# Performance work log

Measured on AMD Instinct MI355X. Metric: run time of the kernel, lower is better.

The kernel has to match this reference:

```python
import jax, jax.numpy as jnp
import numpy as np

DIM_M = 512
NEG_INF = -1e30


def setup_inputs() -> dict:
    key = jax.random.key(0)
    k1, k2, k3, k4, k5, k6, k7 = jax.random.split(key, 7)
    B, Lc, Lq, d = 16, 1024, 512, DIM_M
    C = jax.random.normal(k1, (B, Lc, d), dtype=jnp.float32)
    Q = jax.random.normal(k2, (B, Lq, d), dtype=jnp.float32)
    cmask = jax.random.randint(k3, (B, Lc), 0, 2).astype(jnp.float32)
    qmask = jax.random.randint(k4, (B, Lq), 0, 2).astype(jnp.float32)
    lim = np.sqrt(1.0 / d)
    w = jax.random.uniform(k5, (3 * d,), minval=-lim, maxval=lim, dtype=jnp.float32)
    # out_linear: Linear(4d -> d), torch default init
    bound = np.sqrt(1.0 / (4 * d))
    out_w = jax.random.uniform(k6, (d, 4 * d), minval=-bound, maxval=bound, dtype=jnp.float32)
    out_b = jax.random.uniform(k7, (d,), minval=-bound, maxval=bound, dtype=jnp.float32)
    return {"C": C, "Q": Q, "cmask": cmask, "qmask": qmask, "w": w, "out_w": out_w, "out_b": out_b}


def _mask_logits(t, m):
    return t * m + (1.0 - m) * NEG_INF


def reference(C, Q, cmask, qmask, w, out_w, out_b):
    d = C.shape[-1]
    w1, w2, w3 = w[:d], w[d:2 * d], w[2 * d:]
    # Decomposed trilinear similarity (same math as cat([Ct,Qt,Ct*Qt]) @ w):
    # S[b,i,j] = C[b,i]@w1 + Q[b,j]@w2 + (C[b,i]*w3) @ Q[b,j]
    S = (C @ w1)[:, :, None] + (Q @ w2)[:, None, :] \
        + jnp.einsum('bid,bjd->bij', C * w3, Q)  # [B, Lc, Lq]
    qm = qmask[:, None, :]  # [B, 1, Lq]
    cm = cmask[:, :, None]  # [B, Lc, 1]
    S1 = jax.nn.softmax(_mask_logits(S, qm), axis=2)  # over Lq
    S2 = jax.nn.softmax(_mask_logits(S, cm), axis=1)  # over Lc
    A = jnp.einsum('bij,bjd->bid', S1, Q)  # [B, Lc, d]
    # bmm(bmm(S1, S2^T), C) == S1 @ (S2^T @ C) by associativity (cheaper)
    S2TC = jnp.einsum('bij,bid->bjd', S2, C)  # [B, Lq, d]
    Bm = jnp.einsum('bij,bjd->bid', S1, S2TC)  # [B, Lc, d]
    out = jnp.concatenate([C, A, C * A, C * Bm], axis=2)  # [B, Lc, 4d]
    # dropout inactive (inference); out_linear
    return out @ out_w.T + out_b
```

## Files before the change

kernel.cpp:

```cpp
#include <hip/hip_runtime.h>
#include <hip/hip_bf16.h>


#define NB 16
#define LC 1024
#define LQ 512
#define DM 512
#define D4 2048
#define NEGINF (-1e30f)

typedef __bf16 v8bf __attribute__((ext_vector_type(8)));
typedef __bf16 v4bf __attribute__((ext_vector_type(4)));
typedef float  v4f  __attribute__((ext_vector_type(4)));

#define MFMA16 __builtin_amdgcn_mfma_f32_16x16x32_bf16

#define GLOAD16(gp, lp) __builtin_amdgcn_global_load_lds( \
    (const __attribute__((address_space(1))) void*)(gp), \
    (__attribute__((address_space(3))) void*)(lp), 16, 0, 0)

__device__ __forceinline__ void xcd_remap(int& bx, int& by, int& bz) {
  const int gx = gridDim.x, gy = gridDim.y, gz = gridDim.z;
  int flat = bx + gx * (by + gy * bz);
  int per = (gx * gy * gz) >> 3;
  int nw = (flat & 7) * per + (flat >> 3);
  bx = nw % gx;
  int r = nw / gx;
  by = r % gy;
  bz = r / gy;
}

#define P_PROLOG \
  __shared__ __bf16 Al[4][128 * 32], Bl[4][64 * 32]; \
  int bx = blockIdx.x, by = blockIdx.y, bz = blockIdx.z; \
  xcd_remap(bx, by, bz); \
  const int b = bz, i0 = by * 128, n0 = bx * 64; \
  const int t = threadIdx.x, lane = t & 63, wave = t >> 6; \
  const int wm = wave >> 1, wn = wave & 1, quad = lane >> 4, col = lane & 15; \
  const int srA = wave * 32 + (lane >> 2); \
  const int srB = wave * 16 + (lane >> 2); \
  const int swz = (((lane & 3) ^ ((lane >> 2) & 3) ^ ((lane >> 4) & 3)) * 8); \
  const int rdx = ((quad ^ (col & 3) ^ ((col >> 2) & 3)) * 8); \
  v4f acc[4][2]; \
  _Pragma("unroll") for (int x = 0; x < 4; ++x) \
  _Pragma("unroll") for (int y = 0; y < 2; ++y) \
  _Pragma("unroll") for (int r = 0; r < 4; ++r) acc[x][y][r] = 0.f;

#define P_STAGE1(s, Aptr, Bptr, LDGA, LDGB, k0) \
  do { \
    GLOAD16((Aptr) + (k0),                       &Al[s][(wave * 32) * 32]); \
    GLOAD16((Aptr) + (size_t)16 * (LDGA) + (k0), &Al[s][(wave * 32 + 16) * 32]); \
    GLOAD16((Bptr) + (k0),                       &Bl[s][(wave * 16) * 32]); \
  } while (0)

#define P_COMPUTE(buf) \
  do { \
    v8bf af_[4], bf_[2]; \
    _Pragma("unroll") for (int x = 0; x < 4; ++x) \
      af_[x] = *(const v8bf*)&Al[buf][(wm * 64 + x * 16 + col) * 32 + rdx]; \
    _Pragma("unroll") for (int y = 0; y < 2; ++y) \
      bf_[y] = *(const v8bf*)&Bl[buf][(wn * 32 + y * 16 + col) * 32 + rdx]; \
    _Pragma("unroll") for (int x = 0; x < 4; ++x) \
    _Pragma("unroll") for (int y = 0; y < 2; ++y) \
      acc[x][y] = MFMA16(af_[x], bf_[y], acc[x][y], 0, 0, 0); \
  } while (0)

#define P_KLOOP(Arow, Brow, LDGA, LDGB, KEXT) \
  { P_STAGE1(0, Arow, Brow, LDGA, LDGB, 0); \
    P_STAGE1(1, Arow, Brow, LDGA, LDGB, 32); \
    const int np_ = (KEXT) / 64; \
    for (int q = 0; q < np_; ++q) { \
      asm volatile("s_waitcnt vmcnt(0)" ::: "memory"); \
      __builtin_amdgcn_s_barrier(); \
      const int s0_ = (2 * q) & 3, s1_ = s0_ + 1; \
      if (q + 1 < np_) { \
        const int t0_ = (2 * q + 2) & 3, t1_ = t0_ + 1; \
        P_STAGE1(t0_, Arow, Brow, LDGA, LDGB, (q + 1) * 64); \
        P_STAGE1(t1_, Arow, Brow, LDGA, LDGB, (q + 1) * 64 + 32); \
      } \
      P_COMPUTE(s0_); \
      P_COMPUTE(s1_); \
    } }

#define O_PROLOG \
  __shared__ __bf16 Al[3][128 * 32], Bl[3][128 * 32]; \
  int bx = blockIdx.x, by = blockIdx.y, bz = blockIdx.z; \
  xcd_remap(bx, by, bz); \
  const int b = bz, i0 = by * 128, n0 = bx * 128; \
  const int t = threadIdx.x, lane = t & 63, wave = t >> 6; \
  const int wm = wave >> 1, wn = wave & 1, quad = lane >> 4, col = lane & 15; \
  const int sr32 = wave * 32 + (lane >> 2); \
  const int swz = (((lane & 3) ^ ((lane >> 2) & 3) ^ ((lane >> 4) & 3)) * 8); \
  const int rdx = ((quad ^ (col & 3) ^ ((col >> 2) & 3)) * 8); \
  v4f acc[4][4]; \
  _Pragma("unroll") for (int x = 0; x < 4; ++x) \
  _Pragma("unroll") for (int y = 0; y < 4; ++y) \
  _Pragma("unroll") for (int r = 0; r < 4; ++r) acc[x][y][r] = 0.f;

#define O_STAGE(buf, Aptr, Bptr, LDGA, LDGB, k0) \
  do { \
    GLOAD16((Aptr) + (k0),                       &Al[buf][(wave * 32) * 32]); \
    GLOAD16((Aptr) + (size_t)16 * (LDGA) + (k0), &Al[buf][(wave * 32 + 16) * 32]); \
    GLOAD16((Bptr) + (k0),                       &Bl[buf][(wave * 32) * 32]); \
    GLOAD16((Bptr) + (size_t)16 * (LDGB) + (k0), &Bl[buf][(wave * 32 + 16) * 32]); \
  } while (0)

#define O_COMPUTE(buf) \
  do { \
    v8bf af_[4], bf_[4]; \
    _Pragma("unroll") for (int x = 0; x < 4; ++x) \
      af_[x] = *(const v8bf*)&Al[buf][(wm * 64 + x * 16 + col) * 32 + rdx]; \
    _Pragma("unroll") for (int y = 0; y < 4; ++y) \
      bf_[y] = *(const v8bf*)&Bl[buf][(wn * 64 + y * 16 + col) * 32 + rdx]; \
    __builtin_amdgcn_s_setprio(1); \
    _Pragma("unroll") for (int x = 0; x < 4; ++x) \
    _Pragma("unroll") for (int y = 0; y < 4; ++y) \
      acc[x][y] = MFMA16(af_[x], bf_[y], acc[x][y], 0, 0, 0); \
    __builtin_amdgcn_s_setprio(0); \
  } while (0)

#define O_SYNC4() \
  do { asm volatile("s_waitcnt vmcnt(4)" ::: "memory"); \
       __builtin_amdgcn_s_barrier(); } while (0)
#define O_SYNC0() \
  do { asm volatile("s_waitcnt vmcnt(0)" ::: "memory"); \
       __builtin_amdgcn_s_barrier(); } while (0)

#define O_ROT() do { cur_ = (cur_ == 2) ? 0 : cur_ + 1; \
                     nx2_ = (nx2_ == 2) ? 0 : nx2_ + 1; } while (0)

__global__ void k_rowdots(const float* __restrict__ C, const float* __restrict__ Q,
                          const float* __restrict__ w,
                          float* __restrict__ cw1, float* __restrict__ qw2,
                          __bf16* __restrict__ Cbf, __bf16* __restrict__ Qw3) {
  const int wid = threadIdx.x >> 6, lane = threadIdx.x & 63;
  const int row = blockIdx.x * 4 + wid;
  const bool isC = row < NB * LC;
  const int lr = isC ? row : row - NB * LC;
  const float* src = (isC ? C : Q) + (size_t)lr * DM;
  const float* wv  = isC ? w : (w + DM);
  const float* w3  = w + 2 * DM;
  __bf16* dst = (isC ? Cbf : Qw3) + (size_t)lr * DM;
  float v = 0.f;
#pragma unroll
  for (int s = 0; s < 2; ++s) {
    const int k = lane * 4 + s * 256;
    float4 f = *(const float4*)(src + k);
    float4 g = *(const float4*)(wv + k);
    v += f.x * g.x + f.y * g.y + f.z * g.z + f.w * g.w;
    v4bf h;
    if (isC) {
      h[0] = (__bf16)f.x; h[1] = (__bf16)f.y; h[2] = (__bf16)f.z; h[3] = (__bf16)f.w;
    } else {
      float4 s3 = *(const float4*)(w3 + k);
      h[0] = (__bf16)(f.x * s3.x); h[1] = (__bf16)(f.y * s3.y);
      h[2] = (__bf16)(f.z * s3.z); h[3] = (__bf16)(f.w * s3.w);
    }
    *(v4bf*)(dst + k) = h;
  }
#pragma unroll
  for (int off = 32; off; off >>= 1) v += __shfl_down(v, off, 64);
  if (lane == 0) {
    if (isC) cw1[row] = v;
    else     qw2[lr] = v;
  }
}

__device__ __forceinline__ void transpose_tile_f32(const float* __restrict__ in,
                                                   __bf16* __restrict__ outT,
                                                   int R, int Cd, int tbx, int tby, int tb) {
  __shared__ __bf16 tile[64][66];
  const int r0 = tby * 64, c0 = tbx * 64;
  const int tr = threadIdx.x >> 6, tc = threadIdx.x & 63;
  const float* inb = in + (size_t)tb * R * Cd;
  __bf16* outb = outT + (size_t)tb * Cd * R;
  for (int r = tr; r < 64; r += 4)
    tile[r][tc] = (__bf16)inb[(size_t)(r0 + r) * Cd + c0 + tc];
  __syncthreads();
  for (int c = tr; c < 64; c += 4)
    outb[(size_t)(c0 + c) * R + r0 + tc] = tile[tc][c];
}

__device__ __forceinline__ void transpose_tile_bf(const __bf16* __restrict__ in,
                                                  __bf16* __restrict__ outT,
                                                  int R, int Cd, int tbx, int tby, int tb) {
  __shared__ __bf16 tile[64][66];
  const int r0 = tby * 64, c0 = tbx * 64;
  const int tr = threadIdx.x >> 6, tc = threadIdx.x & 63;
  const __bf16* inb = in + (size_t)tb * R * Cd;
  __bf16* outb = outT + (size_t)tb * Cd * R;
  for (int r = tr; r < 64; r += 4)
    tile[r][tc] = inb[(size_t)(r0 + r) * Cd + c0 + tc];
  __syncthreads();
  for (int c = tr; c < 64; c += 4)
    outb[(size_t)(c0 + c) * R + r0 + tc] = tile[tc][c];
}

__global__ void k_prep(const float* __restrict__ C, const __bf16* __restrict__ Cbf,
                       const float* __restrict__ Q, const float* __restrict__ OW,
                       __bf16* __restrict__ CT, __bf16* __restrict__ QT,
                       __bf16* __restrict__ OWb, int use_cbf) {
  const int id = blockIdx.x;
  if (id < 2048) {
    if (use_cbf) transpose_tile_bf(Cbf, CT, LC, DM, id & 7, (id >> 3) & 15, id >> 7);
    else         transpose_tile_f32(C,  CT, LC, DM, id & 7, (id >> 3) & 15, id >> 7);
  } else if (id < 3072) {
    const int id2 = id - 2048;
    transpose_tile_f32(Q, QT, LQ, DM, id2 & 7, (id2 >> 3) & 7, id2 >> 6);
  } else {
    const size_t i = ((size_t)(id - 3072) * 256 + threadIdx.x) * 4;
    float4 f = *(const float4*)(OW + i);
    v4bf h; h[0] = (__bf16)f.x; h[1] = (__bf16)f.y; h[2] = (__bf16)f.z; h[3] = (__bf16)f.w;
    *(v4bf*)(OWb + i) = h;
  }
}

__global__ void k_cvt2b(const float* __restrict__ Cf, const float* __restrict__ OW,
                        __bf16* __restrict__ Cb3, __bf16* __restrict__ OWb) {
  const size_t NC = (size_t)NB * LC * DM;
  size_t i = ((size_t)blockIdx.x * 256 + threadIdx.x) * 4;
  if (i < NC) {
    float4 f = *(const float4*)(Cf + i);
    v4bf h; h[0] = (__bf16)f.x; h[1] = (__bf16)f.y; h[2] = (__bf16)f.z; h[3] = (__bf16)f.w;
    *(v4bf*)(Cb3 + i) = h;
  } else {
    size_t j = i - NC;
    float4 f = *(const float4*)(OW + j);
    v4bf h; h[0] = (__bf16)f.x; h[1] = (__bf16)f.y; h[2] = (__bf16)f.z; h[3] = (__bf16)f.w;
    *(v4bf*)(OWb + j) = h;
  }
}

__global__ __launch_bounds__(256) void k_mfma_S(
    const __bf16* __restrict__ Cbf, const __bf16* __restrict__ Qw3,
    const float* __restrict__ cw1, const float* __restrict__ qw2,
    float* __restrict__ S) {
  P_PROLOG
  const __bf16* Arow = Cbf + (size_t)b * LC * DM + (size_t)(i0 + srA) * DM + swz;
  const __bf16* Brow = Qw3 + (size_t)b * LQ * DM + (size_t)(n0 + srB) * DM + swz;
  P_KLOOP(Arow, Brow, DM, DM, DM)
  float* Sb = S + (size_t)b * LC * LQ;
#pragma unroll
  for (int x = 0; x < 4; ++x) {
    const int mB = i0 + wm * 64 + x * 16 + quad * 4;
    float cv[4];
#pragma unroll
    for (int r = 0; r < 4; ++r) cv[r] = cw1[b * LC + mB + r];
#pragma unroll
    for (int y = 0; y < 2; ++y) {
      const int j = n0 + wn * 32 + y * 16 + col;
      const float qv = qw2[b * LQ + j];
#pragma unroll
      for (int r = 0; r < 4; ++r)
        Sb[(size_t)(mB + r) * LQ + j] = acc[x][y][r] + cv[r] + qv;
    }
  }
}

__global__ __launch_bounds__(1024) void k_softstat(
    const float* __restrict__ S, const float* __restrict__ qmask,
    const float* __restrict__ cmask, __bf16* __restrict__ S1,
    float2* __restrict__ pstat) {
  __shared__ float2 cst[16][LQ];
  const int b = blockIdx.y, ic = blockIdx.x;
  const int tid = threadIdx.x, wv = tid >> 6, lane = tid & 63;
  const float* qm  = qmask + b * LQ;
  const float* cm  = cmask + b * LC + ic * 64;
  const float* Sb  = S  + ((size_t)b * LC + ic * 64) * LQ;
  __bf16*      S1b = S1 + ((size_t)b * LC + ic * 64) * LQ;
  float colm[8], cols[8];
#pragma unroll
  for (int tt = 0; tt < 8; ++tt) { colm[tt] = -3e38f; cols[tt] = 0.f; }
  for (int it = 0; it < 4; ++it) {
    const int r = wv * 4 + it;
    const float cmv = cm[r];
    const float* Srow = Sb + (size_t)r * LQ;
    float sv[8], l1[8];
    float m = -3e38f;
#pragma unroll
    for (int tt = 0; tt < 8; ++tt) {
      int j = lane + 64 * tt;
      sv[tt] = Srow[j];
      float qv = qm[j];
      l1[tt] = qv * sv[tt] + (1.f - qv) * NEGINF;
      m = fmaxf(m, l1[tt]);
    }
#pragma unroll
    for (int off = 32; off; off >>= 1) m = fmaxf(m, __shfl_xor(m, off, 64));
    float e[8], s = 0.f;
#pragma unroll
    for (int tt = 0; tt < 8; ++tt) { e[tt] = __expf(l1[tt] - m); s += e[tt]; }
#pragma unroll
    for (int off = 32; off; off >>= 1) s += __shfl_xor(s, off, 64);
    const float inv = 1.f / s;
#pragma unroll
    for (int tt = 0; tt < 8; ++tt)
      S1b[(size_t)r * LQ + lane + 64 * tt] = (__bf16)(e[tt] * inv);
    if (cmv != 0.f) {
#pragma unroll
      for (int tt = 0; tt < 8; ++tt) {
        float l2 = sv[tt];
        if (l2 > colm[tt]) { cols[tt] *= __expf(colm[tt] - l2); colm[tt] = l2; }
        cols[tt] += __expf(l2 - colm[tt]);
      }
    }
  }
#pragma unroll
  for (int tt = 0; tt < 8; ++tt) cst[wv][lane + 64 * tt] = make_float2(colm[tt], cols[tt]);
  __syncthreads();
  if (tid < LQ) {
    float M = -3e38f, Sd = 0.f;
#pragma unroll
    for (int k = 0; k < 16; ++k) {
      float2 p = cst[k][tid];
      float nM = fmaxf(M, p.x);
      Sd = Sd * __expf(M - nM) + p.y * __expf(p.x - nM);
      M = nM;
    }
    pstat[((size_t)(b * 16 + ic) * LQ) + tid] = make_float2(M, Sd);
  }
}

__global__ void k_colwrite(const float* __restrict__ S, const float* __restrict__ cmask,
                           const float2* __restrict__ pstat, __bf16* __restrict__ S2T) {
  __shared__ float Mf[64], If[64];
  __shared__ __bf16 tile[64][66];
  const int b = blockIdx.z, ic = blockIdx.y, j0 = blockIdx.x * 64;
  const int c = threadIdx.x & 63, ip = threadIdx.x >> 6;
  if (threadIdx.x < 64) {
    float M = -3e38f, Sd = 0.f;
#pragma unroll
    for (int k = 0; k < 16; ++k) {
      float2 p = pstat[((size_t)(b * 16 + k) * LQ) + j0 + threadIdx.x];
      float nM = fmaxf(M, p.x);
      Sd = Sd * __expf(M - nM) + p.y * __expf(p.x - nM);
      M = nM;
    }
    Mf[threadIdx.x] = M; If[threadIdx.x] = 1.f / Sd;
  }
  __syncthreads();
  const float M = Mf[c], inv = If[c];
  const float* Sb = S + ((size_t)b * LC + ic * 64) * LQ;
  const float* cm = cmask + b * LC + ic * 64;
  for (int r = ip; r < 64; r += 4) {
    if (cm[r] != 0.f)
      tile[r][c] = (__bf16)(__expf(Sb[(size_t)r * LQ + j0 + c] - M) * inv);
    else
      tile[r][c] = (__bf16)0.f;
  }
  __syncthreads();
  __bf16* S2Tb = S2T + ((size_t)b * LQ + j0) * LC + ic * 64;
  for (int jr = ip; jr < 64; jr += 4)
    S2Tb[(size_t)jr * LC + c] = tile[c][jr];
}

__global__ __launch_bounds__(256) void k_mfma_A(
    const __bf16* __restrict__ S1, const __bf16* __restrict__ QT,
    const float* __restrict__ Cf, const __bf16* __restrict__ Cbfp, int use_cbf,
    __bf16* __restrict__ Aw, __bf16* __restrict__ CAw) {
  P_PROLOG
  const __bf16* Arow = S1 + (size_t)b * LC * LQ + (size_t)(i0 + srA) * LQ + swz;
  const __bf16* Brow = QT + (size_t)b * DM * LQ + (size_t)(n0 + srB) * LQ + swz;
  P_KLOOP(Arow, Brow, LQ, LQ, LQ)
  __bf16* Ab  = Aw  + (size_t)b * LC * DM;
  __bf16* CAb = CAw + (size_t)b * LC * DM;
  if (use_cbf) {
    const __bf16* Cb = Cbfp + (size_t)b * LC * DM;
#pragma unroll
    for (int x = 0; x < 4; ++x) {
      const int mB = i0 + wm * 64 + x * 16 + quad * 4;
#pragma unroll
      for (int y = 0; y < 2; ++y) {
        const int n = n0 + wn * 32 + y * 16 + col;
#pragma unroll
        for (int r = 0; r < 4; ++r) {
          const float av = acc[x][y][r];
          const float cv = (float)Cb[(size_t)(mB + r) * DM + n];
          Ab[(size_t)(mB + r) * DM + n]  = (__bf16)av;
          CAb[(size_t)(mB + r) * DM + n] = (__bf16)(av * cv);
        }
      }
    }
  } else {
    const float* Cb = Cf + (size_t)b * LC * DM;
#pragma unroll
    for (int x = 0; x < 4; ++x) {
      const int mB = i0 + wm * 64 + x * 16 + quad * 4;
#pragma unroll
      for (int y = 0; y < 2; ++y) {
        const int n = n0 + wn * 32 + y * 16 + col;
#pragma unroll
        for (int r = 0; r < 4; ++r) {
          const float av = acc[x][y][r];
          const float cv = Cb[(size_t)(mB + r) * DM + n];
          Ab[(size_t)(mB + r) * DM + n]  = (__bf16)av;
          CAb[(size_t)(mB + r) * DM + n] = (__bf16)(av * cv);
        }
      }
    }
  }
}

__global__ __launch_bounds__(256) void k_mfma_T(
    const __bf16* __restrict__ S2T, const __bf16* __restrict__ CT, __bf16* __restrict__ S2TCT) {
  P_PROLOG
  const int j0 = i0;
  const __bf16* Arow = S2T + (size_t)b * LQ * LC + (size_t)(j0 + srA) * LC + swz;
  const __bf16* Brow = CT  + (size_t)b * DM * LC + (size_t)(n0 + srB) * LC + swz;
  P_KLOOP(Arow, Brow, LC, LC, LC)
#pragma unroll
  for (int x = 0; x < 4; ++x) {
    const int jB = j0 + wm * 64 + x * 16 + quad * 4;
#pragma unroll
    for (int y = 0; y < 2; ++y) {
      const int n = n0 + wn * 32 + y * 16 + col;
      v4bf h;
#pragma unroll
      for (int r = 0; r < 4; ++r) h[r] = (__bf16)acc[x][y][r];
      *(v4bf*)&S2TCT[((size_t)b * DM + n) * LQ + jB] = h;
    }
  }
}

__global__ __launch_bounds__(256) void k_mfma_Bm(
    const __bf16* __restrict__ S1, const __bf16* __restrict__ S2TCT,
    const float* __restrict__ Cf, const __bf16* __restrict__ Cbfp, int use_cbf,
    __bf16* __restrict__ CBw) {
  P_PROLOG
  const __bf16* Arow = S1    + (size_t)b * LC * LQ + (size_t)(i0 + srA) * LQ + swz;
  const __bf16* Brow = S2TCT + (size_t)b * DM * LQ + (size_t)(n0 + srB) * LQ + swz;
  P_KLOOP(Arow, Brow, LQ, LQ, LQ)
  __bf16* CBb = CBw + (size_t)b * LC * DM;
  if (use_cbf) {
    const __bf16* Cb = Cbfp + (size_t)b * LC * DM;
#pragma unroll
    for (int x = 0; x < 4; ++x) {
      const int mB = i0 + wm * 64 + x * 16 + quad * 4;
#pragma unroll
      for (int y = 0; y < 2; ++y) {
        const int n = n0 + wn * 32 + y * 16 + col;
#pragma unroll
        for (int r = 0; r < 4; ++r) {
          const float cv = (float)Cb[(size_t)(mB + r) * DM + n];
          CBb[(size_t)(mB + r) * DM + n] = (__bf16)(acc[x][y][r] * cv);
        }
      }
    }
  } else {
    const float* Cb = Cf + (size_t)b * LC * DM;
#pragma unroll
    for (int x = 0; x < 4; ++x) {
      const int mB = i0 + wm * 64 + x * 16 + quad * 4;
#pragma unroll
      for (int y = 0; y < 2; ++y) {
        const int n = n0 + wn * 32 + y * 16 + col;
#pragma unroll
        for (int r = 0; r < 4; ++r) {
          const float cv = Cb[(size_t)(mB + r) * DM + n];
          CBb[(size_t)(mB + r) * DM + n] = (__bf16)(acc[x][y][r] * cv);
        }
      }
    }
  }
}

__global__ __launch_bounds__(256) void k_mfma_out(
    const __bf16* __restrict__ Cb3, const __bf16* __restrict__ Aw,
    const __bf16* __restrict__ CAw, const __bf16* __restrict__ CBw,
    const __bf16* __restrict__ OWb, const float* __restrict__ ob,
    float* __restrict__ out) {
  O_PROLOG
  const size_t rowoff = (size_t)b * LC * DM + (size_t)(i0 + sr32) * DM + swz;
  const __bf16* Aseg[4] = {Cb3 + rowoff, Aw + rowoff, CAw + rowoff, CBw + rowoff};
  const __bf16* Brow0 = OWb + (size_t)(n0 + sr32) * D4 + swz;
  O_STAGE(0, Aseg[0], Brow0, DM, D4, 0);
  O_STAGE(1, Aseg[0], Brow0, DM, D4, 32);
  O_SYNC4();
  int cur_ = 0, nx2_ = 2;
#pragma unroll
  for (int seg = 0; seg < 4; ++seg) {
    const __bf16* Ac = Aseg[seg];
    const __bf16* An = Aseg[seg < 3 ? seg + 1 : 3];
    const __bf16* Bc = Brow0 + seg * DM;
    const __bf16* Bn = Brow0 + (seg < 3 ? seg + 1 : 3) * DM;
    for (int j = 0; j < 14; ++j) {
      O_STAGE(nx2_, Ac, Bc, DM, D4, (j + 2) * 32);
      O_COMPUTE(cur_);
      O_SYNC4();
      O_ROT();
    }
    if (seg < 3) {
      O_STAGE(nx2_, An, Bn, DM, D4, 0);
      O_COMPUTE(cur_);
      O_SYNC4();
      O_ROT();
      O_STAGE(nx2_, An, Bn, DM, D4, 32);
      O_COMPUTE(cur_);
      O_SYNC4();
      O_ROT();
    } else {
      O_COMPUTE(cur_);
      O_SYNC0();
      O_ROT();
      O_COMPUTE(cur_);
    }
  }
  float* outb = out + (size_t)b * LC * DM;
#pragma unroll
  for (int x = 0; x < 4; ++x) {
    const int mB = i0 + wm * 64 + x * 16 + quad * 4;
#pragma unroll
    for (int y = 0; y < 4; ++y) {
      const int n = n0 + wn * 64 + y * 16 + col;
      const float bv = ob[n];
#pragma unroll
      for (int r = 0; r < 4; ++r)
        outb[(size_t)(mB + r) * DM + n] = acc[x][y][r] + bv;
    }
  }
}

extern "C" void kernel_launch(void* const* d_in, const int* in_sizes, int n_in,
                              void* d_out, int out_size, void* d_ws, size_t ws_size,
                              hipStream_t stream) {
  const float* C     = (const float*)d_in[0];
  const float* Q     = (const float*)d_in[1];
  const float* cmask = (const float*)d_in[2];
  const float* qmask = (const float*)d_in[3];
  const float* w     = (const float*)d_in[4];
  const float* out_w = (const float*)d_in[5];
  const float* out_b = (const float*)d_in[6];
  float* out = (float*)d_out;

  char* base = (char*)d_ws;
  float*  cw1   = (float*)base;
  float*  qw2   = (float*)(base + 65536);
  char*   R     = base + 131072;
  float*  S     = (float*)R;
  __bf16* CT    = (__bf16*)R;
  __bf16* Aw    = (__bf16*)R;
  __bf16* QT    = (__bf16*)(R + (16u << 20));
  __bf16* CBw   = (__bf16*)(R + (16u << 20));
  __bf16* S1    = (__bf16*)(R + (32u << 20));
  __bf16* Qw3   = (__bf16*)(R + (48u << 20));
  __bf16* S2T   = (__bf16*)(R + (48u << 20));
  __bf16* CAw   = (__bf16*)(R + (48u << 20));
  float2* pstat = (float2*)(R + (64u << 20));
  __bf16* S2TCT = (__bf16*)(R + (64u << 20));
  (void)in_sizes; (void)n_in; (void)out_size;

  const size_t need_big = 131072 + (90ull << 20);
  const bool bigws = ws_size >= need_big;

  __bf16 *Cbf, *Cbf3, *OWbf;
  if (bigws) {
    Cbf  = (__bf16*)(R + (72u << 20));
    Cbf3 = Cbf;
    OWbf = (__bf16*)(R + (88u << 20));
  } else {
    Cbf  = (__bf16*)(R + (32u << 20));
    Cbf3 = (__bf16*)(R + (32u << 20));
    OWbf = (__bf16*)(R + (64u << 20));
  }
  const int ucb = bigws ? 1 : 0;

  k_rowdots<<<(NB * LC + NB * LQ) / 4, 256, 0, stream>>>(C, Q, w, cw1, qw2, Cbf, Qw3);
  k_mfma_S<<<dim3(LQ / 64, LC / 128, NB), 256, 0, stream>>>(Cbf, Qw3, cw1, qw2, S);
  k_softstat<<<dim3(LC / 64, NB), 1024, 0, stream>>>(S, qmask, cmask, S1, pstat);
  k_colwrite<<<dim3(LQ / 64, LC / 64, NB), 256, 0, stream>>>(S, cmask, pstat, S2T);
  k_prep<<<bigws ? 4096 : 3072, 256, 0, stream>>>(C, Cbf, Q, out_w, CT, QT, OWbf, ucb);
  k_mfma_T<<<dim3(DM / 64, LQ / 128, NB), 256, 0, stream>>>(S2T, CT, S2TCT);
  k_mfma_A<<<dim3(DM / 64, LC / 128, NB), 256, 0, stream>>>(S1, QT, C, Cbf3, ucb, Aw, CAw);
  k_mfma_Bm<<<dim3(DM / 64, LC / 128, NB), 256, 0, stream>>>(S1, S2TCT, C, Cbf3, ucb, CBw);
  if (!bigws)
    k_cvt2b<<<(NB * LC * DM + DM * D4) / 1024, 256, 0, stream>>>(C, out_w, Cbf3, OWbf);
  k_mfma_out<<<dim3(DM / 128, LC / 128, NB), 256, 0, stream>>>(Cbf3, Aw, CAw, CBw, OWbf, out_b, out);
}
```

Before: 277.6 us.

## Fuse A and Bm GEMMs sharing S1 tiles, switch P k-loop to triple buffering

Adds a fused kernel that computes S1@Q and S1@S2TC together, loading each S1 tile once and writing A, C*A and C*Bm in one epilogue. It runs only when the workspace is large enough to hold a separate CBw buffer. The shared P-style k-loop moves from a 4-slot, two-stage scheme to a 3-slot rotating pipeline with partial vmcnt waits. The output GEMM drops its setprio hints. The fused kernel doubles accumulator registers and uses more LDS, which may lower occupancy, and its benefit depends on the harness workspace size.

Measured after the change: 275.4 us. Within noise of the previous version (-0.8%).

```diff
diff --git a/kernel.cpp b/kernel.cpp
--- a/kernel.cpp
+++ b/kernel.cpp
@@ -31,7 +31,7 @@
 }
 
 #define P_PROLOG \
-  __shared__ __bf16 Al[4][128 * 32], Bl[4][64 * 32]; \
+  __shared__ __bf16 Al[3][128 * 32], Bl[3][64 * 32]; \
   int bx = blockIdx.x, by = blockIdx.y, bz = blockIdx.z; \
   xcd_remap(bx, by, bz); \
   const int b = bz, i0 = by * 128, n0 = bx * 64; \
@@ -46,11 +46,11 @@
   _Pragma("unroll") for (int y = 0; y < 2; ++y) \
   _Pragma("unroll") for (int r = 0; r < 4; ++r) acc[x][y][r] = 0.f;
 
-#define P_STAGE1(s, Aptr, Bptr, LDGA, LDGB, k0) \
+#define P_STAGE(buf, Aptr, Bptr, LDGA, LDGB, k0) \
   do { \
-    GLOAD16((Aptr) + (k0),                       &Al[s][(wave * 32) * 32]); \
-    GLOAD16((Aptr) + (size_t)16 * (LDGA) + (k0), &Al[s][(wave * 32 + 16) * 32]); \
-    GLOAD16((Bptr) + (k0),                       &Bl[s][(wave * 16) * 32]); \
+    GLOAD16((Aptr) + (k0),                       &Al[buf][(wave * 32) * 32]); \
+    GLOAD16((Aptr) + (size_t)16 * (LDGA) + (k0), &Al[buf][(wave * 32 + 16) * 32]); \
+    GLOAD16((Bptr) + (k0),                       &Bl[buf][(wave * 16) * 32]); \
   } while (0)
 
 #define P_COMPUTE(buf) \
@@ -65,21 +65,34 @@
       acc[x][y] = MFMA16(af_[x], bf_[y], acc[x][y], 0, 0, 0); \
   } while (0)
 
+#define P_SYNC3() \
+  do { asm volatile("s_waitcnt vmcnt(3)" ::: "memory"); \
+       __builtin_amdgcn_s_barrier(); } while (0)
+#define P_SYNC0() \
+  do { asm volatile("s_waitcnt vmcnt(0)" ::: "memory"); \
+       __builtin_amdgcn_s_barrier(); } while (0)
+
+#define P_ROT() do { cur_ = (cur_ == 2) ? 0 : cur_ + 1; \
+                     nx2_ = (nx2_ == 2) ? 0 : nx2_ + 1; } while (0)
+
 #define P_KLOOP(Arow, Brow, LDGA, LDGB, KEXT) \
-  { P_STAGE1(0, Arow, Brow, LDGA, LDGB, 0); \
-    P_STAGE1(1, Arow, Brow, LDGA, LDGB, 32); \
-    const int np_ = (KEXT) / 64; \
-    for (int q = 0; q < np_; ++q) { \
-      asm volatile("s_waitcnt vmcnt(0)" ::: "memory"); \
-      __builtin_amdgcn_s_barrier(); \
-      const int s0_ = (2 * q) & 3, s1_ = s0_ + 1; \
-      if (q + 1 < np_) { \
-        const int t0_ = (2 * q + 2) & 3, t1_ = t0_ + 1; \
-        P_STAGE1(t0_, Arow, Brow, LDGA, LDGB, (q + 1) * 64); \
-        P_STAGE1(t1_, Arow, Brow, LDGA, LDGB, (q + 1) * 64 + 32); \
+  { P_STAGE(0, Arow, Brow, LDGA, LDGB, 0); \
+    P_STAGE(1, Arow, Brow, LDGA, LDGB, 32); \
+    P_SYNC3(); \
+    int cur_ = 0, nx2_ = 2; \
+    for (int k0 = 0; k0 < (KEXT); k0 += 32) { \
+      const int kn_ = k0 + 64; \
+      if (kn_ < (KEXT)) { \
+        P_STAGE(nx2_, Arow, Brow, LDGA, LDGB, kn_); \
+        P_COMPUTE(cur_); \
+        P_SYNC3(); \
+      } else if (k0 + 32 < (KEXT)) { \
+        P_COMPUTE(cur_); \
+        P_SYNC0(); \
+      } else { \
+        P_COMPUTE(cur_); \
       } \
-      P_COMPUTE(s0_); \
-      P_COMPUTE(s1_); \
+      P_ROT(); \
     } }
 
 #define O_PROLOG \
@@ -112,11 +125,9 @@
       af_[x] = *(const v8bf*)&Al[buf][(wm * 64 + x * 16 + col) * 32 + rdx]; \
     _Pragma("unroll") for (int y = 0; y < 4; ++y) \
       bf_[y] = *(const v8bf*)&Bl[buf][(wn * 64 + y * 16 + col) * 32 + rdx]; \
-    __builtin_amdgcn_s_setprio(1); \
     _Pragma("unroll") for (int x = 0; x < 4; ++x) \
     _Pragma("unroll") for (int y = 0; y < 4; ++y) \
       acc[x][y] = MFMA16(af_[x], bf_[y], acc[x][y], 0, 0, 0); \
-    __builtin_amdgcn_s_setprio(0); \
   } while (0)
 
 #define O_SYNC4() \
@@ -464,6 +475,103 @@
   }
 }
 
+__global__ __launch_bounds__(256) void k_mfma_AB(
+    const __bf16* __restrict__ S1, const __bf16* __restrict__ QT,
+    const __bf16* __restrict__ S2TCT, const __bf16* __restrict__ Cbfp,
+    __bf16* __restrict__ Aw, __bf16* __restrict__ CAw, __bf16* __restrict__ CBw) {
+  __shared__ __bf16 Al[3][128 * 32], BlQ[3][64 * 32], BlS[3][64 * 32];
+  int bx = blockIdx.x, by = blockIdx.y, bz = blockIdx.z;
+  xcd_remap(bx, by, bz);
+  const int b = bz, i0 = by * 128, n0 = bx * 64;
+  const int t = threadIdx.x, lane = t & 63, wave = t >> 6;
+  const int wm = wave >> 1, wn = wave & 1, quad = lane >> 4, col = lane & 15;
+  const int srA = wave * 32 + (lane >> 2);
+  const int srB = wave * 16 + (lane >> 2);
+  const int swz = (((lane & 3) ^ ((lane >> 2) & 3) ^ ((lane >> 4) & 3)) * 8);
+  const int rdx = ((quad ^ (col & 3) ^ ((col >> 2) & 3)) * 8);
+  v4f accA[4][2], accB[4][2];
+#pragma unroll
+  for (int x = 0; x < 4; ++x)
+#pragma unroll
+    for (int y = 0; y < 2; ++y)
+#pragma unroll
+      for (int r = 0; r < 4; ++r) { accA[x][y][r] = 0.f; accB[x][y][r] = 0.f; }
+  const __bf16* Arow  = S1    + (size_t)b * LC * LQ + (size_t)(i0 + srA) * LQ + swz;
+  const __bf16* BrowQ = QT    + (size_t)b * DM * LQ + (size_t)(n0 + srB) * LQ + swz;
+  const __bf16* BrowS = S2TCT + (size_t)b * DM * LQ + (size_t)(n0 + srB) * LQ + swz;
+
+#define AB_STAGE(buf, k0) \
+  do { \
+    GLOAD16(Arow + (k0),                      &Al[buf][(wave * 32) * 32]); \
+    GLOAD16(Arow + (size_t)16 * LQ + (k0),    &Al[buf][(wave * 32 + 16) * 32]); \
+    GLOAD16(BrowQ + (k0),                     &BlQ[buf][(wave * 16) * 32]); \
+    GLOAD16(BrowS + (k0),                     &BlS[buf][(wave * 16) * 32]); \
+  } while (0)
+
+#define AB_COMPUTE(buf) \
+  do { \
+    v8bf af_[4], bq_[2], bs_[2]; \
+    _Pragma("unroll") for (int x = 0; x < 4; ++x) \
+      af_[x] = *(const v8bf*)&Al[buf][(wm * 64 + x * 16 + col) * 32 + rdx]; \
+    _Pragma("unroll") for (int y = 0; y < 2; ++y) { \
+      bq_[y] = *(const v8bf*)&BlQ[buf][(wn * 32 + y * 16 + col) * 32 + rdx]; \
+      bs_[y] = *(const v8bf*)&BlS[buf][(wn * 32 + y * 16 + col) * 32 + rdx]; \
+    } \
+    _Pragma("unroll") for (int x = 0; x < 4; ++x) \
+    _Pragma("unroll") for (int y = 0; y < 2; ++y) { \
+      accA[x][y] = MFMA16(af_[x], bq_[y], accA[x][y], 0, 0, 0); \
+      accB[x][y] = MFMA16(af_[x], bs_[y], accB[x][y], 0, 0, 0); \
+    } \
+  } while (0)
+
+  AB_STAGE(0, 0);
+  AB_STAGE(1, 32);
+  asm volatile("s_waitcnt vmcnt(4)" ::: "memory");
+  __builtin_amdgcn_s_barrier();
+  int cur_ = 0, nx2_ = 2;
+  for (int k0 = 0; k0 < LQ; k0 += 32) {
+    const int kn_ = k0 + 64;
+    if (kn_ < LQ) {
+      AB_STAGE(nx2_, kn_);
+      AB_COMPUTE(cur_);
+      asm volatile("s_waitcnt vmcnt(4)" ::: "memory");
+      __builtin_amdgcn_s_barrier();
+    } else if (k0 + 32 < LQ) {
+      AB_COMPUTE(cur_);
+      asm volatile("s_waitcnt vmcnt(0)" ::: "memory");
+      __builtin_amdgcn_s_barrier();
+    } else {
+      AB_COMPUTE(cur_);
+    }
+    cur_ = (cur_ == 2) ? 0 : cur_ + 1;
+    nx2_ = (nx2_ == 2) ? 0 : nx2_ + 1;
+  }
+#undef AB_STAGE
+#undef AB_COMPUTE
+
+  __bf16* Ab  = Aw  + (size_t)b * LC * DM;
+  __bf16* CAb = CAw + (size_t)b * LC * DM;
+  __bf16* CBb = CBw + (size_t)b * LC * DM;
+  const __bf16* Cb = Cbfp + (size_t)b * LC * DM;
+#pragma unroll
+  for (int x = 0; x < 4; ++x) {
+    const int mB = i0 + wm * 64 + x * 16 + quad * 4;
+#pragma unroll
+    for (int y = 0; y < 2; ++y) {
+      const int n = n0 + wn * 32 + y * 16 + col;
+#pragma unroll
+      for (int r = 0; r < 4; ++r) {
+        const float av = accA[x][y][r];
+        const float bv = accB[x][y][r];
+        const float cv = (float)Cb[(size_t)(mB + r) * DM + n];
+        Ab[(size_t)(mB + r) * DM + n]  = (__bf16)av;
+        CAb[(size_t)(mB + r) * DM + n] = (__bf16)(av * cv);
+        CBb[(size_t)(mB + r) * DM + n] = (__bf16)(bv * cv);
+      }
+    }
+  }
+}
+
 __global__ __launch_bounds__(256) void k_mfma_out(
     const __bf16* __restrict__ Cb3, const __bf16* __restrict__ Aw,
     const __bf16* __restrict__ CAw, const __bf16* __restrict__ CBw,
@@ -540,7 +648,6 @@
   __bf16* CT    = (__bf16*)R;
   __bf16* Aw    = (__bf16*)R;
   __bf16* QT    = (__bf16*)(R + (16u << 20));
-  __bf16* CBw   = (__bf16*)(R + (16u << 20));
   __bf16* S1    = (__bf16*)(R + (32u << 20));
   __bf16* Qw3   = (__bf16*)(R + (48u << 20));
   __bf16* S2T   = (__bf16*)(R + (48u << 20));
@@ -549,10 +656,10 @@
   __bf16* S2TCT = (__bf16*)(R + (64u << 20));
   (void)in_sizes; (void)n_in; (void)out_size;
 
-  const size_t need_big = 131072 + (90ull << 20);
-  const bool bigws = ws_size >= need_big;
-
-  __bf16 *Cbf, *Cbf3, *OWbf;
+  const bool bigws = ws_size >= 131072 + (90ull << 20);
+  const bool tier3 = ws_size >= 131072 + (106ull << 20);
+
+  __bf16 *Cbf, *Cbf3, *OWbf, *CBw;
   if (bigws) {
     Cbf  = (__bf16*)(R + (72u << 20));
     Cbf3 = Cbf;
@@ -562,6 +669,8 @@
     Cbf3 = (__bf16*)(R + (32u << 20));
     OWbf = (__bf16*)(R + (64u << 20));
   }
+  CBw = tier3 ? (__bf16*)(R + (90u << 20))
+              : (__bf16*)(R + (16u << 20));
   const int ucb = bigws ? 1 : 0;
 
   k_rowdots<<<(NB * LC + NB * LQ) / 4, 256, 0, stream>>>(C, Q, w, cw1, qw2, Cbf, Qw3);
@@ -570,8 +679,13 @@
   k_colwrite<<<dim3(LQ / 64, LC / 64, NB), 256, 0, stream>>>(S, cmask, pstat, S2T);
   k_prep<<<bigws ? 4096 : 3072, 256, 0, stream>>>(C, Cbf, Q, out_w, CT, QT, OWbf, ucb);
   k_mfma_T<<<dim3(DM / 64, LQ / 128, NB), 256, 0, stream>>>(S2T, CT, S2TCT);
-  k_mfma_A<<<dim3(DM / 64, LC / 128, NB), 256, 0, stream>>>(S1, QT, C, Cbf3, ucb, Aw, CAw);
-  k_mfma_Bm<<<dim3(DM / 64, LC / 128, NB), 256, 0, stream>>>(S1, S2TCT, C, Cbf3, ucb, CBw);
+  if (tier3) {
+    k_mfma_AB<<<dim3(DM / 64, LC / 128, NB), 256, 0, stream>>>(
+        S1, QT, S2TCT, Cbf, Aw, CAw, CBw);
+  } else {
+    k_mfma_A<<<dim3(DM / 64, LC / 128, NB), 256, 0, stream>>>(S1, QT, C, Cbf3, ucb, Aw, CAw);
+    k_mfma_Bm<<<dim3(DM / 64, LC / 128, NB), 256, 0, stream>>>(S1, S2TCT, C, Cbf3, ucb, CBw);
+  }
   if (!bigws)
     k_cvt2b<<<(NB * LC * DM + DM * D4) / 1024, 256, 0, stream>>>(C, out_w, Cbf3, OWbf);
   k_mfma_out<<<dim3(DM / 128, LC / 128, NB), 256, 0, stream>>>(Cbf3, Aw, CAw, CBw, OWbf, out_b, out);
```
